# Optimization experiments

Measured on AMD Instinct MI355X. Metric: run time of the kernel, lower is better.

The kernel has to match this reference:

```python
import jax, jax.numpy as jnp
import numpy as np
import math

B_TOPK = 8  # self.B
NEG = -1e9  # numerically-equivalent stand-in for float('-inf') mask


def setup_inputs() -> dict:
    key = jax.random.key(0)
    ks = jax.random.split(key, 12)
    b, s, d, d_low = 4, 2048, 128, 16
    sc = 1.0 / math.sqrt(d)
    return {
        "queries": jax.random.normal(ks[0], (b, s, d), jnp.float32),
        "keys": jax.random.normal(ks[1], (b, s, d), jnp.float32),
        "values": jax.random.normal(ks[2], (b, s, d), jnp.float32),
        "valid_lens": jax.random.randint(ks[3], (b, s), 0, s, jnp.int32),
        "Wq_low": jax.random.normal(ks[4], (d, d_low), jnp.float32) * sc,
        "bq_low": jnp.zeros((d_low,), jnp.float32),
        "Wk_low": jax.random.normal(ks[5], (d, d_low), jnp.float32) * sc,
        "bk_low": jnp.zeros((d_low,), jnp.float32),
        "Wq_high": jax.random.normal(ks[6], (d, d_low), jnp.float32) * sc,
        "bq_high": jnp.zeros((d_low,), jnp.float32),
        "Wk_high": jax.random.normal(ks[7], (d, d_low), jnp.float32) * sc,
        "bk_high": jnp.zeros((d_low,), jnp.float32),
    }


def reference(queries, keys, values, valid_lens, Wq_low, bq_low, Wk_low, bk_low,
              Wq_high, bq_high, Wk_high, bk_high):
    b, s, d = queries.shape
    d_low = Wq_low.shape[1]
    scale = 1.0 / math.sqrt(d_low)

    # low-rank scores [b, sq, sk]
    q_low = queries @ Wq_low + bq_low
    k_low = keys @ Wk_low + bk_low
    scores_low = jnp.einsum('bqe,bke->bqk', q_low, k_low) * scale

    # mask: scatter -inf at (batch, valid_lens[b,k], k) along dim 1 (as in torch code)
    vl = jnp.clip(valid_lens, 0, s - 1)                      # [b, sk]
    mask = vl[:, None, :] == jnp.arange(s)[None, :, None]    # [b, sq, sk]
    scores_masked = jnp.where(mask, scores_low + NEG, scores_low)

    # top-B keys per query row (over key axis)
    _, topk_idx = jax.lax.top_k(scores_masked, B_TOPK)       # [b, s, B]

    # gather top-B queries/keys per row, project to d_low, rank-d_low correction score
    bi = jnp.arange(b)[:, None, None]
    q_high = queries[bi, topk_idx]                           # [b, s, B, d]
    k_high = keys[bi, topk_idx]                              # [b, s, B, d]
    q_proj = q_high @ Wq_high + bq_high                      # [b, s, B, d_low]
    k_proj = k_high @ Wk_high + bk_high
    score_high = jnp.sum(q_proj * k_proj, axis=-1) * scale   # [b, s, B]

    # scatter corrected scores back into the masked score matrix (dim 2)
    si = jnp.arange(s)[None, :, None]
    corrected = scores_masked.at[bi, si, topk_idx].set(score_high)

    # masked_softmax with valid_lens applies softmax over dim=1
    attn = jax.nn.softmax(corrected, axis=1)
    return jnp.einsum('bqk,bkd->bqd', attn, values)
```

## Files before the change

kernel.cpp:

```cpp
#include <hip/hip_runtime.h>
#include <float.h>
#include <math.h>

#define SEQ 2048
#define NB 4
#define DIM 128
#define DL 16
#define NEGV (-1e9f)
#define TOPK 8

#define QT 128
#define KC 64
#define QCH 64

typedef unsigned long long u64;
typedef __attribute__((ext_vector_type(8))) short short8;
typedef __attribute__((ext_vector_type(4))) float f32x4;

__device__ __forceinline__ void top8_insert(float* s, float key) {
    #pragma unroll
    for (int i = 0; i < 8; ++i) {
        float a = s[i];
        s[i] = fmaxf(a, key);
        key  = fminf(a, key);
    }
}

__device__ __forceinline__ float top8_merge16(float* s) {
    #pragma unroll
    for (int off = 1; off < 16; off <<= 1) {
        float o[8], t[8];
        #pragma unroll
        for (int i = 0; i < 8; ++i)
            o[i] = __shfl_xor(s[i], off, 64);
        #pragma unroll
        for (int i = 0; i < 8; ++i)
            t[i] = fmaxf(s[i], o[7 - i]);
        #pragma unroll
        for (int i = 0; i < 4; ++i) {
            float a = t[i], c = t[i + 4];
            t[i] = fmaxf(a, c); t[i + 4] = fminf(a, c);
        }
        #pragma unroll
        for (int g2 = 0; g2 < 8; g2 += 4) {
            float a = t[g2], c = t[g2 + 2];
            t[g2] = fmaxf(a, c); t[g2 + 2] = fminf(a, c);
            a = t[g2 + 1]; c = t[g2 + 3];
            t[g2 + 1] = fmaxf(a, c); t[g2 + 3] = fminf(a, c);
        }
        #pragma unroll
        for (int g1 = 0; g1 < 8; g1 += 2) {
            float a = t[g1], c = t[g1 + 1];
            t[g1] = fmaxf(a, c); t[g1 + 1] = fminf(a, c);
        }
        #pragma unroll
        for (int i = 0; i < 8; ++i) s[i] = t[i];
    }
    return s[7];
}

__device__ __forceinline__ unsigned bf16_rne(float x) {
    unsigned u = __float_as_uint(x);
    return (u + 0x7FFFu + ((u >> 16) & 1u)) >> 16;
}

__global__ __launch_bounds__(256) void proj_kernel(
    const float* __restrict__ q, const float* __restrict__ k,
    const float* __restrict__ Wql, const float* __restrict__ bql,
    const float* __restrict__ Wkl, const float* __restrict__ bkl,
    const float* __restrict__ Wqh, const float* __restrict__ bqh,
    const float* __restrict__ Wkh, const float* __restrict__ bkh,
    unsigned short* __restrict__ qA1, unsigned short* __restrict__ qA2,
    unsigned short* __restrict__ qA3,
    unsigned short* __restrict__ kB1, unsigned short* __restrict__ kB2,
    float* __restrict__ sh)
{
    __shared__ float Ws[4][DIM * DL];
    __shared__ float rowq[16][DIM];
    __shared__ float rowk[16][DIM];
    int tid = threadIdx.x;
    for (int i = tid; i < DIM * DL; i += 256) {
        Ws[0][i] = Wql[i];
        Ws[1][i] = Wkl[i];
        Ws[2][i] = Wqh[i];
        Ws[3][i] = Wkh[i];
    }
    int r0 = blockIdx.x * 16;
    for (int i = tid; i < 16 * DIM; i += 256) {
        int rr = i >> 7, cc = i & 127;
        rowq[rr][cc] = q[(size_t)(r0 + rr) * DIM + cc];
        rowk[rr][cc] = k[(size_t)(r0 + rr) * DIM + cc];
    }
    __syncthreads();
    int g = tid >> 4;
    int e = tid & 15;
    float aql = 0.f, akl = 0.f, aqh = 0.f, akh = 0.f;
    #pragma unroll 8
    for (int i = 0; i < DIM; ++i) {
        float qv = rowq[g][i], kv = rowk[g][i];
        aql = fmaf(qv, Ws[0][i * DL + e], aql);
        akl = fmaf(kv, Ws[1][i * DL + e], akl);
        aqh = fmaf(qv, Ws[2][i * DL + e], aqh);
        akh = fmaf(kv, Ws[3][i * DL + e], akh);
    }
    int t = r0 + g;
    float qv = aql + bql[e];
    float kv = akl + bkl[e];

    unsigned q1 = bf16_rne(qv);
    float q1f = __uint_as_float(q1 << 16);
    float qr1 = qv - q1f;
    unsigned q2 = bf16_rne(qr1);
    float q2f = __uint_as_float(q2 << 16);
    unsigned q3 = bf16_rne(qr1 - q2f);

    unsigned k1 = bf16_rne(kv);
    float k1f = __uint_as_float(k1 << 16);
    float kr1 = kv - k1f;
    unsigned k2 = bf16_rne(kr1);
    float k2f = __uint_as_float(k2 << 16);
    unsigned k3 = bf16_rne(kr1 - k2f);

    size_t pb = (size_t)t * 32;
    qA1[pb + e] = (unsigned short)q1; qA1[pb + 16 + e] = (unsigned short)q2;
    qA2[pb + e] = (unsigned short)q2; qA2[pb + 16 + e] = (unsigned short)q1;
    qA3[pb + e] = (unsigned short)q1; qA3[pb + 16 + e] = (unsigned short)q3;
    kB1[pb + e] = (unsigned short)k1; kB1[pb + 16 + e] = (unsigned short)k2;
    kB2[pb + e] = (unsigned short)k3; kB2[pb + 16 + e] = (unsigned short)k1;

    float qp = aqh + bqh[e];
    float kp = akh + bkh[e];
    float prod = qp * kp;
    #pragma unroll
    for (int off = 8; off >= 1; off >>= 1)
        prod += __shfl_xor(prod, off, 16);
    if (e == 0) sh[t] = 0.25f * prod;
}

__global__ __launch_bounds__(256) void vsplit_kernel(
    const float* __restrict__ V, unsigned short* __restrict__ VH,
    unsigned short* __restrict__ VL)
{
    __shared__ float T[32][33];
    int kb = blockIdx.x * 32, db = blockIdx.y * 32, b = blockIdx.z;
    int tid = threadIdx.x;
    {
        int r = tid >> 3, cg = tid & 7;
        float4 v = *(const float4*)(V + ((size_t)b * SEQ + kb + r) * DIM + db + cg * 4);
        T[r][cg * 4 + 0] = v.x; T[r][cg * 4 + 1] = v.y;
        T[r][cg * 4 + 2] = v.z; T[r][cg * 4 + 3] = v.w;
    }
    __syncthreads();
    int dr = tid >> 3, kg = tid & 7;
    unsigned h[4], l[4];
    #pragma unroll
    for (int j = 0; j < 4; ++j) {
        float f = T[kg * 4 + j][dr];
        unsigned hi = bf16_rne(f);
        float hf = __uint_as_float(hi << 16);
        unsigned lo = bf16_rne(f - hf);
        h[j] = hi; l[j] = lo;
    }
    size_t o = ((size_t)b * DIM + db + dr) * SEQ + kb + kg * 4;
    *(uint2*)(VH + o) = make_uint2(h[0] | (h[1] << 16), h[2] | (h[3] << 16));
    *(uint2*)(VL + o) = make_uint2(l[0] | (l[1] << 16), l[2] | (l[3] << 16));
}

__global__ __launch_bounds__(256) void score_mfma(
    const unsigned short* __restrict__ qA1, const unsigned short* __restrict__ qA2,
    const unsigned short* __restrict__ qA3,
    const unsigned short* __restrict__ kB1, const unsigned short* __restrict__ kB2,
    const int* __restrict__ valid_lens, const float* __restrict__ sh,
    float* __restrict__ Smat, float2* __restrict__ pml, int do_stats)
{
    __shared__ float red[4][16][8];
    __shared__ float thr_s[16];

    int tid  = threadIdx.x;
    int lane = tid & 63;
    int wv   = tid >> 6;
    int c15  = lane & 15;
    int g    = lane >> 4;
    int row0 = __builtin_amdgcn_readfirstlane(blockIdx.x * 16);
    int b    = row0 >> 11;
    int qi0  = row0 & (SEQ - 1);

    size_t aoff = (size_t)(row0 + c15) * 32 + g * 8;
    short8 A1 = *(const short8*)(qA1 + aoff);
    short8 A2 = *(const short8*)(qA2 + aoff);
    short8 A3 = *(const short8*)(qA3 + aoff);

    const unsigned short* kb1 = kB1 + (size_t)b * SEQ * 32;
    const unsigned short* kb2 = kB2 + (size_t)b * SEQ * 32;
    const int* vlb = valid_lens + (size_t)b * SEQ;

    float s8[4][8];
    #pragma unroll
    for (int r = 0; r < 4; ++r)
        #pragma unroll
        for (int i = 0; i < 8; ++i) s8[r][i] = -FLT_MAX;

    int rowg[4];
    #pragma unroll
    for (int r = 0; r < 4; ++r) rowg[r] = qi0 + g * 4 + r;

    #pragma unroll
    for (int t = 0; t < 32; ++t) {
        int col = (wv * 32 + t) * 16 + c15;
        size_t boff = (size_t)col * 32 + g * 8;
        short8 B1 = *(const short8*)(kb1 + boff);
        short8 B2 = *(const short8*)(kb2 + boff);

        f32x4 acc = (f32x4){0.f, 0.f, 0.f, 0.f};
        acc = __builtin_amdgcn_mfma_f32_16x16x32_bf16(A1, B1, acc, 0, 0, 0);
        acc = __builtin_amdgcn_mfma_f32_16x16x32_bf16(A2, B1, acc, 0, 0, 0);
        acc = __builtin_amdgcn_mfma_f32_16x16x32_bf16(A3, B2, acc, 0, 0, 0);

        int vl = vlb[col];
        vl = vl < 0 ? 0 : (vl > SEQ - 1 ? SEQ - 1 : vl);

        #pragma unroll
        for (int r = 0; r < 4; ++r) {
            float v = 0.25f * acc[r];
            if (vl == rowg[r]) v += NEGV;
            top8_insert(s8[r], v);
        }
    }

    #pragma unroll
    for (int r = 0; r < 4; ++r) top8_merge16(s8[r]);

    if (c15 == 0) {
        #pragma unroll
        for (int r = 0; r < 4; ++r)
            #pragma unroll
            for (int i = 0; i < 8; ++i)
                red[wv][g * 4 + r][i] = s8[r][i];
    }
    __syncthreads();
    if (tid < 16) {
        float fin[8];
        #pragma unroll
        for (int i = 0; i < 8; ++i) fin[i] = red[0][tid][i];
        #pragma unroll
        for (int w2 = 1; w2 < 4; ++w2)
            #pragma unroll
            for (int i = 0; i < 8; ++i)
                top8_insert(fin, red[w2][tid][i]);
        thr_s[tid] = fin[7];
    }
    __syncthreads();

    const float* shb = sh + (size_t)b * SEQ;
    int chunk = qi0 >> 4;
    float thr_l[4];
    #pragma unroll
    for (int r = 0; r < 4; ++r) thr_l[r] = thr_s[g * 4 + r];

    #pragma unroll
    for (int t = 0; t < 32; ++t) {
        int col = (wv * 32 + t) * 16 + c15;
        size_t boff = (size_t)col * 32 + g * 8;
        short8 B1 = *(const short8*)(kb1 + boff);
        short8 B2 = *(const short8*)(kb2 + boff);

        f32x4 acc = (f32x4){0.f, 0.f, 0.f, 0.f};
        acc = __builtin_amdgcn_mfma_f32_16x16x32_bf16(A1, B1, acc, 0, 0, 0);
        acc = __builtin_amdgcn_mfma_f32_16x16x32_bf16(A2, B1, acc, 0, 0, 0);
        acc = __builtin_amdgcn_mfma_f32_16x16x32_bf16(A3, B2, acc, 0, 0, 0);

        int vl = vlb[col];
        vl = vl < 0 ? 0 : (vl > SEQ - 1 ? SEQ - 1 : vl);
        float shk = shb[col];

        float* So = Smat + (size_t)(row0 + g * 4) * SEQ + col;
        float m = -FLT_MAX, l = 0.f;
        #pragma unroll
        for (int r = 0; r < 4; ++r) {
            float v = 0.25f * acc[r];
            if (vl == rowg[r]) v += NEGV;
            v = (v >= thr_l[r]) ? shk : v;
            So[(size_t)r * SEQ] = v;
            float nm = fmaxf(m, v);
            l = l * __expf(m - nm) + __expf(v - nm);
            m = nm;
        }
        if (do_stats) {
            #pragma unroll
            for (int off = 16; off <= 32; off <<= 1) {
                float mo = __shfl_xor(m, off, 64);
                float lo = __shfl_xor(l, off, 64);
                float nm = fmaxf(m, mo);
                l = l * __expf(m - nm) + lo * __expf(mo - nm);
                m = nm;
            }
            if (g == 0)
                pml[((size_t)b * 128 + chunk) * SEQ + col] = make_float2(m, l);
        }
    }
}

__global__ __launch_bounds__(256) void colred_final2(
    const float2* __restrict__ pml,
    float* __restrict__ cmax, float* __restrict__ cinv)
{
    __shared__ float2 red[4][64];
    int tid = threadIdx.x;
    int c0 = tid & 63, sl = tid >> 6;
    int gcol = blockIdx.x * 64 + c0;
    int b = gcol >> 11, kcol = gcol & (SEQ - 1);
    float m = -FLT_MAX, l = 0.f;
    #pragma unroll 8
    for (int i = 0; i < 32; ++i) {
        int c = sl * 32 + i;
        float2 p = pml[((size_t)b * 128 + c) * SEQ + kcol];
        float nm = fmaxf(m, p.x);
        l = l * __expf(m - nm) + p.y * __expf(p.x - nm);
        m = nm;
    }
    red[sl][c0] = make_float2(m, l);
    __syncthreads();
    if (sl == 0) {
        #pragma unroll
        for (int s = 1; s < 4; ++s) {
            float2 p = red[s][c0];
            float nm = fmaxf(m, p.x);
            l = l * __expf(m - nm) + p.y * __expf(p.x - nm);
            m = nm;
        }
        cmax[gcol] = m;
        cinv[gcol] = 1.f / l;
    }
}

__global__ __launch_bounds__(256) void colred_partial(
    const float* __restrict__ Smat, float* __restrict__ pm, float* __restrict__ pl)
{
    int kcol = blockIdx.x * 256 + threadIdx.x;
    int qc = blockIdx.y;
    int b  = blockIdx.z;
    const float* Sp = Smat + (size_t)b * SEQ * SEQ + (size_t)(qc * QCH) * SEQ + kcol;
    float m = -FLT_MAX, l = 0.f;
    #pragma unroll 4
    for (int qq = 0; qq < QCH; ++qq) {
        float v = Sp[(size_t)qq * SEQ];
        float nm = fmaxf(m, v);
        l = l * __expf(m - nm) + __expf(v - nm);
        m = nm;
    }
    pm[((size_t)b * 32 + qc) * SEQ + kcol] = m;
    pl[((size_t)b * 32 + qc) * SEQ + kcol] = l;
}

__global__ __launch_bounds__(256) void colred_final(
    const float* __restrict__ pm, const float* __restrict__ pl,
    float* __restrict__ cmax, float* __restrict__ cinv)
{
    int idx = blockIdx.x * 256 + threadIdx.x;
    int b = idx >> 11, kcol = idx & (SEQ - 1);
    float m = -FLT_MAX, l = 0.f;
    #pragma unroll
    for (int c = 0; c < 32; ++c) {
        float mm = pm[((size_t)b * 32 + c) * SEQ + kcol];
        float ll = pl[((size_t)b * 32 + c) * SEQ + kcol];
        float nm = fmaxf(m, mm);
        l = l * __expf(m - nm) + ll * __expf(mm - nm);
        m = nm;
    }
    cmax[idx] = m;
    cinv[idx] = 1.f / l;
}

__global__ __launch_bounds__(256) void out_mfma(
    const float* __restrict__ Smat, const unsigned short* __restrict__ VH,
    const unsigned short* __restrict__ VL,
    const float* __restrict__ cmax, const float* __restrict__ cinv,
    float* __restrict__ dst, int krange)
{
    __shared__ unsigned int VtH[DIM * 32];
    __shared__ unsigned int VtL[DIM * 32];

    int tid  = threadIdx.x;
    int w    = tid >> 6;
    int lane = tid & 63;
    int ln   = lane & 15;
    int quad = lane >> 4;
    int q0   = blockIdx.x * QT;
    int ksid = blockIdx.y;
    int b    = blockIdx.z;
    int kbeg = ksid * krange;

    const float* Sb = Smat + (size_t)b * SEQ * SEQ;
    const unsigned short* VHb = VH + (size_t)b * DIM * SEQ;
    const unsigned short* VLb = VL + (size_t)b * DIM * SEQ;
    const float* cm  = cmax + (size_t)b * SEQ;
    const float* ci  = cinv + (size_t)b * SEQ;

    f32x4 acc[2][8];
    #pragma unroll
    for (int mt = 0; mt < 2; ++mt)
        #pragma unroll
        for (int nt = 0; nt < 8; ++nt)
            acc[mt][nt] = (f32x4){0.f, 0.f, 0.f, 0.f};

    int sd0   = tid >> 3;
    int skseg = tid & 7;

    for (int k0 = kbeg; k0 < kbeg + krange; k0 += KC) {
        #pragma unroll
        for (int it = 0; it < 4; ++it) {
            int d = sd0 + it * 32;
            size_t go = (size_t)d * SEQ + k0 + skseg * 8;
            uint4 hv = *(const uint4*)(VHb + go);
            uint4 lv = *(const uint4*)(VLb + go);
            int wa = d * 32 + ((skseg ^ (d & 7)) << 2);
            *(uint4*)&VtH[wa] = hv;
            *(uint4*)&VtL[wa] = lv;
        }

        short8 Ah[2][2], Al[2][2];
        #pragma unroll
        for (int ks = 0; ks < 2; ++ks) {
            int kk = k0 + ks * 32 + quad * 8;
            float4 cma = *(const float4*)(cm + kk);
            float4 cmb = *(const float4*)(cm + kk + 4);
            float4 cia = *(const float4*)(ci + kk);
            float4 cib = *(const float4*)(ci + kk + 4);
            #pragma unroll
            for (int mt = 0; mt < 2; ++mt) {
                const float* Sp = Sb + (size_t)(q0 + w * 32 + mt * 16 + ln) * SEQ + kk;
                float4 sa = *(const float4*)Sp;
                float4 sb = *(const float4*)(Sp + 4);
                float p[8];
                p[0] = __expf(sa.x - cma.x) * cia.x;
                p[1] = __expf(sa.y - cma.y) * cia.y;
                p[2] = __expf(sa.z - cma.z) * cia.z;
                p[3] = __expf(sa.w - cma.w) * cia.w;
                p[4] = __expf(sb.x - cmb.x) * cib.x;
                p[5] = __expf(sb.y - cmb.y) * cib.y;
                p[6] = __expf(sb.z - cmb.z) * cib.z;
                p[7] = __expf(sb.w - cmb.w) * cib.w;
                #pragma unroll
                for (int j = 0; j < 8; ++j) {
                    unsigned hi = bf16_rne(p[j]);
                    float hf = __uint_as_float(hi << 16);
                    unsigned lo = bf16_rne(p[j] - hf);
                    Ah[mt][ks][j] = (short)hi;
                    Al[mt][ks][j] = (short)lo;
                }
            }
        }
        __syncthreads();

        #pragma unroll
        for (int nt = 0; nt < 8; ++nt) {
            int d = nt * 16 + ln;
            #pragma unroll
            for (int ks = 0; ks < 2; ++ks) {
                int kseg = ks * 4 + quad;
                int wa = d * 32 + ((kseg ^ (d & 7)) << 2);
                short8 bh = *(short8*)&VtH[wa];
                short8 bl = *(short8*)&VtL[wa];
                #pragma unroll
                for (int mt = 0; mt < 2; ++mt) {
                    acc[mt][nt] = __builtin_amdgcn_mfma_f32_16x16x32_bf16(
                        Ah[mt][ks], bh, acc[mt][nt], 0, 0, 0);
                    acc[mt][nt] = __builtin_amdgcn_mfma_f32_16x16x32_bf16(
                        Al[mt][ks], bh, acc[mt][nt], 0, 0, 0);
                    acc[mt][nt] = __builtin_amdgcn_mfma_f32_16x16x32_bf16(
                        Ah[mt][ks], bl, acc[mt][nt], 0, 0, 0);
                }
            }
        }
        __syncthreads();
    }

    float* dp = dst + (size_t)ksid * ((size_t)NB * SEQ * DIM)
                    + (size_t)b * SEQ * DIM;
    #pragma unroll
    for (int mt = 0; mt < 2; ++mt) {
        #pragma unroll
        for (int r = 0; r < 4; ++r) {
            float* o = dp + (size_t)(q0 + w * 32 + mt * 16 + quad * 4 + r) * DIM + ln;
            #pragma unroll
            for (int nt = 0; nt < 8; ++nt)
                o[nt * 16] = acc[mt][nt][r];
        }
    }
}

__global__ __launch_bounds__(256) void reduce_kernel(
    const float* __restrict__ part, float* __restrict__ out, int ksplit)
{
    int idx = blockIdx.x * 256 + threadIdx.x;
    const float4* p = (const float4*)part;
    float4 a = p[idx];
    for (int s = 1; s < ksplit; ++s) {
        float4 q = p[(size_t)idx + (size_t)s * 262144];
        a.x += q.x; a.y += q.y; a.z += q.z; a.w += q.w;
    }
    ((float4*)out)[idx] = a;
}

extern "C" void kernel_launch(void* const* d_in, const int* in_sizes, int n_in,
                              void* d_out, int out_size, void* d_ws, size_t ws_size,
                              hipStream_t stream)
{
    const float* queries = (const float*)d_in[0];
    const float* keys    = (const float*)d_in[1];
    const float* values  = (const float*)d_in[2];
    const int*   valid   = (const int*)d_in[3];
    const float* Wql = (const float*)d_in[4];
    const float* bql = (const float*)d_in[5];
    const float* Wkl = (const float*)d_in[6];
    const float* bkl = (const float*)d_in[7];
    const float* Wqh = (const float*)d_in[8];
    const float* bqh = (const float*)d_in[9];
    const float* Wkh = (const float*)d_in[10];
    const float* bkh = (const float*)d_in[11];

    char* ws = (char*)d_ws;
    float* Smat = (float*)(ws);
    unsigned short* qA1 = (unsigned short*)(ws + 67108864);
    unsigned short* qA2 = (unsigned short*)(ws + 67633152);
    unsigned short* qA3 = (unsigned short*)(ws + 68157440);
    unsigned short* kB1 = (unsigned short*)(ws + 68681728);
    unsigned short* kB2 = (unsigned short*)(ws + 69206016);
    float* sh    = (float*)(ws + 69730304);
    float* cmax  = (float*)(ws + 69795840);
    float* cinv  = (float*)(ws + 69828608);
    unsigned short* VthH = (unsigned short*)(ws + 69861376);
    unsigned short* VthL = (unsigned short*)(ws + 71958528);
    const size_t part_off = 74055680;
    float2* pml  = (float2*)(ws + part_off);
    float* pm    = (float*)(ws + part_off);
    float* pl    = (float*)(ws + part_off + 1048576);
    float* part  = (float*)(ws + part_off);

    const size_t part_sz  = (size_t)NB * SEQ * DIM * 4;
    int ksplit = 1;
    if      (ws_size >= part_off + 8 * part_sz) ksplit = 8;
    else if (ws_size >= part_off + 4 * part_sz) ksplit = 4;
    else if (ws_size >= part_off + 2 * part_sz) ksplit = 2;

    int fused = (ws_size >= part_off + 8388608) ? 1 : 0;

    proj_kernel<<<dim3((NB * SEQ) / 16), 256, 0, stream>>>(
        queries, keys, Wql, bql, Wkl, bkl, Wqh, bqh, Wkh, bkh,
        qA1, qA2, qA3, kB1, kB2, sh);

    vsplit_kernel<<<dim3(SEQ / 32, DIM / 32, NB), 256, 0, stream>>>(
        values, VthH, VthL);

    score_mfma<<<dim3((NB * SEQ) / 16), 256, 0, stream>>>(
        qA1, qA2, qA3, kB1, kB2, valid, sh, Smat, pml, fused);

    if (fused) {
        colred_final2<<<dim3((NB * SEQ) / 64), 256, 0, stream>>>(pml, cmax, cinv);
    } else {
        colred_partial<<<dim3(SEQ / 256, 32, NB), 256, 0, stream>>>(Smat, pm, pl);
        colred_final<<<dim3((NB * SEQ) / 256), 256, 0, stream>>>(pm, pl, cmax, cinv);
    }

    if (ksplit == 1) {
        out_mfma<<<dim3(SEQ / QT, 1, NB), 256, 0, stream>>>(
            Smat, VthH, VthL, cmax, cinv, (float*)d_out, SEQ);
    } else {
        out_mfma<<<dim3(SEQ / QT, ksplit, NB), 256, 0, stream>>>(
            Smat, VthH, VthL, cmax, cinv, part, SEQ / ksplit);
        reduce_kernel<<<(NB * SEQ * DIM / 4) / 256, 256, 0, stream>>>(
            part, (float*)d_out, ksplit);
    }
}
```

Baseline: 168.5 us.

## Fold column softmax final reduction into output kernel and simplify per-tile stats

The column max/sum reduction over the 128 partial chunks moves into the prologue of out_mfma, which keeps the per-column max and inverse-sum in shared memory. That removes the colred_final2 launch and the global cmax/cinv round trip when the workspace is large enough. In score_mfma the online per-row softmax update is replaced by a single max over four values followed by one sum of exponentials, which cuts the number of exp calls. In exchange, every out_mfma block (one per q-tile) recomputes the 128-chunk reduction for its key range, which repeats that work 16 times, and shared memory use grows by 16KB.

```diff
diff --git a/kernel.cpp b/kernel.cpp
--- a/kernel.cpp
+++ b/kernel.cpp
@@ -274,18 +274,19 @@
         float shk = shb[col];
 
         float* So = Smat + (size_t)(row0 + g * 4) * SEQ + col;
-        float m = -FLT_MAX, l = 0.f;
+        float e[4];
         #pragma unroll
         for (int r = 0; r < 4; ++r) {
             float v = 0.25f * acc[r];
             if (vl == rowg[r]) v += NEGV;
             v = (v >= thr_l[r]) ? shk : v;
             So[(size_t)r * SEQ] = v;
-            float nm = fmaxf(m, v);
-            l = l * __expf(m - nm) + __expf(v - nm);
-            m = nm;
+            e[r] = v;
         }
         if (do_stats) {
+            float m = fmaxf(fmaxf(e[0], e[1]), fmaxf(e[2], e[3]));
+            float l = __expf(e[0] - m) + __expf(e[1] - m)
+                    + __expf(e[2] - m) + __expf(e[3] - m);
             #pragma unroll
             for (int off = 16; off <= 32; off <<= 1) {
                 float mo = __shfl_xor(m, off, 64);
@@ -375,10 +376,13 @@
     const float* __restrict__ Smat, const unsigned short* __restrict__ VH,
     const unsigned short* __restrict__ VL,
     const float* __restrict__ cmax, const float* __restrict__ cinv,
-    float* __restrict__ dst, int krange)
+    const float2* __restrict__ pml,
+    float* __restrict__ dst, int krange, int infinal)
 {
     __shared__ unsigned int VtH[DIM * 32];
     __shared__ unsigned int VtL[DIM * 32];
+    __shared__ float cmx[2048];
+    __shared__ float cin[2048];
 
     int tid  = threadIdx.x;
     int w    = tid >> 6;
@@ -393,8 +397,27 @@
     const float* Sb = Smat + (size_t)b * SEQ * SEQ;
     const unsigned short* VHb = VH + (size_t)b * DIM * SEQ;
     const unsigned short* VLb = VL + (size_t)b * DIM * SEQ;
-    const float* cm  = cmax + (size_t)b * SEQ;
-    const float* ci  = cinv + (size_t)b * SEQ;
+
+    if (infinal) {
+        int col = kbeg + tid;
+        const float2* pp = pml + (size_t)b * 128 * SEQ + col;
+        float m = -FLT_MAX, l = 0.f;
+        #pragma unroll 8
+        for (int c = 0; c < 128; ++c) {
+            float2 p = pp[(size_t)c * SEQ];
+            float nm = fmaxf(m, p.x);
+            l = l * __expf(m - nm) + p.y * __expf(p.x - nm);
+            m = nm;
+        }
+        cmx[tid] = m;
+        cin[tid] = 1.f / l;
+    } else {
+        for (int i = tid; i < krange; i += 256) {
+            cmx[i] = cmax[(size_t)b * SEQ + kbeg + i];
+            cin[i] = cinv[(size_t)b * SEQ + kbeg + i];
+        }
+    }
+    __syncthreads();
 
     f32x4 acc[2][8];
     #pragma unroll
@@ -421,11 +444,12 @@
         short8 Ah[2][2], Al[2][2];
         #pragma unroll
         for (int ks = 0; ks < 2; ++ks) {
-            int kk = k0 + ks * 32 + quad * 8;
-            float4 cma = *(const float4*)(cm + kk);
-            float4 cmb = *(const float4*)(cm + kk + 4);
-            float4 cia = *(const float4*)(ci + kk);
-            float4 cib = *(const float4*)(ci + kk + 4);
+            int kk   = k0 + ks * 32 + quad * 8;
+            int kloc = kk - kbeg;
+            float4 cma = *(const float4*)(cmx + kloc);
+            float4 cmb = *(const float4*)(cmx + kloc + 4);
+            float4 cia = *(const float4*)(cin + kloc);
+            float4 cib = *(const float4*)(cin + kloc + 4);
             #pragma unroll
             for (int mt = 0; mt < 2; ++mt) {
                 const float* Sp = Sb + (size_t)(q0 + w * 32 + mt * 16 + ln) * SEQ + kk;
@@ -531,19 +555,32 @@
     float* cinv  = (float*)(ws + 69828608);
     unsigned short* VthH = (unsigned short*)(ws + 69861376);
     unsigned short* VthL = (unsigned short*)(ws + 71958528);
+
     const size_t part_off = 74055680;
-    float2* pml  = (float2*)(ws + part_off);
-    float* pm    = (float*)(ws + part_off);
-    float* pl    = (float*)(ws + part_off + 1048576);
-    float* part  = (float*)(ws + part_off);
-
+    const size_t pml_sz   = 8388608;
     const size_t part_sz  = (size_t)NB * SEQ * DIM * 4;
-    int ksplit = 1;
-    if      (ws_size >= part_off + 8 * part_sz) ksplit = 8;
-    else if (ws_size >= part_off + 4 * part_sz) ksplit = 4;
-    else if (ws_size >= part_off + 2 * part_sz) ksplit = 2;
-
-    int fused = (ws_size >= part_off + 8388608) ? 1 : 0;
+
+    int fused = 0, infinal = 0, ksplit = 1;
+    float2* pml = (float2*)(ws + part_off);
+    float*  part = (float*)(ws + part_off);
+    float*  pm = (float*)(ws + part_off);
+    float*  pl = (float*)(ws + part_off + 1048576);
+
+    if (ws_size >= part_off + pml_sz + 8 * part_sz) {
+        fused = 1; infinal = 1; ksplit = 8;
+        pml  = (float2*)(ws + part_off);
+        part = (float*)(ws + part_off + pml_sz);
+    } else if (ws_size >= part_off + pml_sz) {
+        fused = 1; infinal = 0;
+        if      (ws_size >= part_off + 8 * part_sz) ksplit = 8;
+        else if (ws_size >= part_off + 4 * part_sz) ksplit = 4;
+        else if (ws_size >= part_off + 2 * part_sz) ksplit = 2;
+    } else {
+        fused = 0; infinal = 0;
+        if      (ws_size >= part_off + 8 * part_sz) ksplit = 8;
+        else if (ws_size >= part_off + 4 * part_sz) ksplit = 4;
+        else if (ws_size >= part_off + 2 * part_sz) ksplit = 2;
+    }
 
     proj_kernel<<<dim3((NB * SEQ) / 16), 256, 0, stream>>>(
         queries, keys, Wql, bql, Wkl, bkl, Wqh, bqh, Wkh, bkh,
@@ -556,7 +593,8 @@
         qA1, qA2, qA3, kB1, kB2, valid, sh, Smat, pml, fused);
 
     if (fused) {
-        colred_final2<<<dim3((NB * SEQ) / 64), 256, 0, stream>>>(pml, cmax, cinv);
+        if (!infinal)
+            colred_final2<<<dim3((NB * SEQ) / 64), 256, 0, stream>>>(pml, cmax, cinv);
     } else {
         colred_partial<<<dim3(SEQ / 256, 32, NB), 256, 0, stream>>>(Smat, pm, pl);
         colred_final<<<dim3((NB * SEQ) / 256), 256, 0, stream>>>(pm, pl, cmax, cinv);
@@ -564,10 +602,10 @@
 
     if (ksplit == 1) {
         out_mfma<<<dim3(SEQ / QT, 1, NB), 256, 0, stream>>>(
-            Smat, VthH, VthL, cmax, cinv, (float*)d_out, SEQ);
+            Smat, VthH, VthL, cmax, cinv, pml, (float*)d_out, SEQ, 0);
     } else {
         out_mfma<<<dim3(SEQ / QT, ksplit, NB), 256, 0, stream>>>(
-            Smat, VthH, VthL, cmax, cinv, part, SEQ / ksplit);
+            Smat, VthH, VthL, cmax, cinv, pml, part, SEQ / ksplit, infinal);
         reduce_kernel<<<(NB * SEQ * DIM / 4) / 256, 256, 0, stream>>>(
             part, (float*)d_out, ksplit);
     }
```

Result: slower. 173.6 us (+3.0%).
